# Kernel optimization log

Hardware: AMD Instinct MI355X
Metric: run time of the kernel (lower is better)

Reference implementation:

```python
import jax, jax.numpy as jnp
import numpy as np

B, CIN, COUT, H, W = 4, 256, 64, 64, 64


def setup_inputs() -> dict:
    key = jax.random.key(0)
    ks = jax.random.split(key, 9)
    s_in = 1.0 / np.sqrt(CIN)
    s_out = 1.0 / np.sqrt(COUT)
    return {
        "x": jax.random.normal(ks[0], (B, CIN, H, W), dtype=jnp.float32),
        "wq": jax.random.uniform(ks[1], (COUT, CIN), jnp.float32, -s_in, s_in),
        "bq": jax.random.uniform(ks[2], (COUT,), jnp.float32, -s_in, s_in),
        "wk": jax.random.uniform(ks[3], (COUT, CIN), jnp.float32, -s_in, s_in),
        "bk": jax.random.uniform(ks[4], (COUT,), jnp.float32, -s_in, s_in),
        "wv": jax.random.uniform(ks[5], (COUT, CIN), jnp.float32, -s_in, s_in),
        "bv": jax.random.uniform(ks[6], (COUT,), jnp.float32, -s_in, s_in),
        "wo": jax.random.uniform(ks[7], (CIN, COUT), jnp.float32, -s_out, s_out),
        "bo": jax.random.uniform(ks[8], (CIN,), jnp.float32, -s_out, s_out),
    }


def reference(x, wq, bq, wk, bk, wv, bv, wo, bo):
    b, f, h, w = x.shape
    xf = x.reshape(b, f, h * w)  # [b, f, hw]
    # 1x1-conv projections (conv2d k=1 == channel-wise linear), flattened to [b, c, hw]
    q = jnp.einsum("bfd,cf->bcd", xf, wq) + bq[None, :, None]
    k = jnp.einsum("bfd,cf->bcd", xf, wk) + bk[None, :, None]
    v = jnp.einsum("bfd,cf->bcd", xf, wv) + bv[None, :, None]
    # full spatial correlation [b, hw, hw], contracting channels (einsum 'bcd,bef->bdf')
    correl = jnp.einsum("bcd,bce->bde", q, k)
    correl = jax.nn.softmax(correl, axis=-1)
    # value @ correl -> [b, c, hw]
    o = jnp.einsum("bcd,bde->bce", v, correl)
    o = o.reshape(b, -1, h, w)
    # output 1x1 conv back to in_channels
    out = jnp.einsum("bchw,fc->bfhw", o, wo) + bo[None, :, None, None]
    return out
```

## Files before the change

### kernel.cpp

```cpp
#include <hip/hip_runtime.h>
#include <hip/hip_bf16.h>

#define BB 4
#define CIN 256
#define CO 64
#define HW_ 4096
#define SPLIT_A 8
#define SPLIT_S 8
#define DCHUNK_A (HW_ / SPLIT_A)
#define ECHUNK_S (HW_ / SPLIT_S)

typedef __attribute__((ext_vector_type(8))) short short8;
typedef __attribute__((ext_vector_type(4))) float f32x4;
typedef __attribute__((ext_vector_type(16))) float f32x16;
typedef __attribute__((ext_vector_type(4))) unsigned uint4v;
typedef __attribute__((ext_vector_type(2))) unsigned uint2v;

__device__ inline unsigned short f2bf(float f) {
  union { float f; unsigned u; } x; x.f = f;
  unsigned r = x.u + 0x7fffu + ((x.u >> 16) & 1u);
  return (unsigned short)(r >> 16);
}
__device__ inline float bf2f(unsigned short h) {
  union { unsigned u; float f; } x; x.u = ((unsigned)h) << 16;
  return x.f;
}
__device__ inline unsigned packbf2(float a, float b) {
  __hip_bfloat162 t = __float22bfloat162_rn(float2{a, b});
  union { __hip_bfloat162 h; unsigned u; } c; c.h = t; return c.u;
}
__device__ inline void gl_lds16(const void* g, void* l) {
  __builtin_amdgcn_global_load_lds(
      (const __attribute__((address_space(1))) unsigned int*)g,
      (__attribute__((address_space(3))) unsigned int*)l, 16, 0, 0);
}

__global__ __launch_bounds__(256, 3) void qkv_kernel(
    const float* __restrict__ x,
    const float* __restrict__ wq, const float* __restrict__ bq,
    const float* __restrict__ wk, const float* __restrict__ bk,
    const float* __restrict__ wv, const float* __restrict__ bv,
    unsigned short* __restrict__ qT, unsigned short* __restrict__ kT,
    unsigned short* __restrict__ v)
{
  const int b = blockIdx.z;
  const int which = blockIdx.y;
  const int n0 = blockIdx.x * 64;
  const int tid = threadIdx.x;
  const int w = tid >> 6, lane = tid & 63;
  const int lq = lane & 15, quad = lane >> 4;

  const float* W  = (which == 0) ? wq : (which == 1) ? wk : wv;
  const float* Bb = (which == 0) ? bq : (which == 1) ? bk : bv;

  __shared__ unsigned short w_lds[64 * 256];
  unsigned char* wbytes = reinterpret_cast<unsigned char*>(w_lds);

#pragma unroll
  for (int i = 0; i < 16; ++i) {
    int L = i * 256 + tid;
    int row = L >> 6, col4 = L & 63;
    float4 w4 = *reinterpret_cast<const float4*>(&W[row * 256 + col4 * 4]);
    ushort4 p;
    p.x = f2bf(w4.x); p.y = f2bf(w4.y); p.z = f2bf(w4.z); p.w = f2bf(w4.w);
    int addr = (row * 512 + col4 * 8) ^ ((row & 7) << 4);
    *reinterpret_cast<ushort4*>(wbytes + addr) = p;
  }
  __syncthreads();

  const int n = n0 + w * 16 + lq;
  const float* xb = x + (size_t)b * CIN * HW_ + n;

  const f32x4 zero = {0.f, 0.f, 0.f, 0.f};
  f32x4 acc[4];
#pragma unroll
  for (int mt = 0; mt < 4; ++mt) acc[mt] = zero;

  for (int ks = 0; ks < 8; ++ks) {
    float xv[8];
#pragma unroll
    for (int j = 0; j < 8; ++j)
      xv[j] = xb[(size_t)(ks * 32 + quad * 8 + j) * HW_];
    short8 bhi, blo;
#pragma unroll
    for (int j = 0; j < 8; ++j) {
      unsigned short h = f2bf(xv[j]);
      bhi[j] = (short)h;
      blo[j] = (short)f2bf(xv[j] - bf2f(h));
    }
#pragma unroll
    for (int mt = 0; mt < 4; ++mt) {
      int addr = ((mt * 16 + lq) * 512 + ks * 64 + quad * 16) ^ ((lq & 7) << 4);
      short8 af = *reinterpret_cast<const short8*>(wbytes + addr);
      acc[mt] = __builtin_amdgcn_mfma_f32_16x16x32_bf16(af, bhi, acc[mt], 0, 0, 0);
      acc[mt] = __builtin_amdgcn_mfma_f32_16x16x32_bf16(af, blo, acc[mt], 0, 0, 0);
    }
  }

  float4 bias4[4];
#pragma unroll
  for (int mt = 0; mt < 4; ++mt)
    bias4[mt] = *reinterpret_cast<const float4*>(&Bb[mt * 16 + quad * 4]);

  if (which < 2) {
    unsigned short* outp = ((which == 0) ? qT : kT) + ((size_t)b * HW_ + n) * 64;
#pragma unroll
    for (int mt = 0; mt < 4; ++mt) {
      ushort4 p;
      p.x = f2bf(acc[mt][0] + bias4[mt].x);
      p.y = f2bf(acc[mt][1] + bias4[mt].y);
      p.z = f2bf(acc[mt][2] + bias4[mt].z);
      p.w = f2bf(acc[mt][3] + bias4[mt].w);
      *reinterpret_cast<ushort4*>(&outp[mt * 16 + quad * 4]) = p;
    }
  } else {
#pragma unroll
    for (int mt = 0; mt < 4; ++mt) {
      float bb[4] = {bias4[mt].x, bias4[mt].y, bias4[mt].z, bias4[mt].w};
#pragma unroll
      for (int r = 0; r < 4; ++r)
        v[((size_t)b * CO + mt * 16 + quad * 4 + r) * HW_ + n] = f2bf(acc[mt][r] + bb[r]);
    }
  }
}

__global__ __launch_bounds__(256, 3) void stats_kernel(
    const unsigned short* __restrict__ qT,
    const unsigned short* __restrict__ kT,
    float2* __restrict__ parts)
{
  const int id = blockIdx.x;
  const int sw = (id & 7) * 128 + (id >> 3);
  const int dtile = sw & 31;
  const int esplit = (sw >> 5) & 7;
  const int b = sw >> 8;
  const int tid = threadIdx.x;
  const int w = tid >> 6, lane = tid & 63;
  const int lo = lane & 31, h = lane >> 5;

  __shared__ __align__(16) unsigned char k_lds[128 * 128];

  const size_t base = (size_t)b * HW_ * CO;
  const int d0 = dtile * 128 + w * 32;

  short8 qf[4];
#pragma unroll
  for (int ks = 0; ks < 4; ++ks)
    qf[ks] = *reinterpret_cast<const short8*>(&qT[base + (size_t)(d0 + lo) * 64 + ks * 16 + h * 8]);

  float m_run = -3.0e38f, l_run = 0.f;
  const char* kT_bytes = reinterpret_cast<const char*>(kT) + base * 2;
  const int e_beg = esplit * ECHUNK_S;

  for (int eb = e_beg; eb < e_beg + ECHUNK_S; eb += 128) {
#pragma unroll
    for (int j = 0; j < 4; ++j) {
      int chunk = w * 4 + j;
      int row = chunk * 8 + (lane >> 3);
      int cp = (lane & 7) * 16;
      gl_lds16(kT_bytes + (size_t)(eb + row) * 128 + (cp ^ ((row & 7) << 4)),
               k_lds + chunk * 1024);
    }
    __syncthreads();

#pragma unroll
    for (int et = 0; et < 4; ++et) {
      const int er = et * 32 + lo;
      f32x16 T;
#pragma unroll
      for (int i = 0; i < 16; ++i) T[i] = 0.f;
#pragma unroll
      for (int ks = 0; ks < 4; ++ks) {
        const short8 kfr = *reinterpret_cast<const short8*>(
            k_lds + er * 128 + ((ks * 32 + h * 16) ^ ((er & 7) << 4)));
        T = __builtin_amdgcn_mfma_f32_32x32x16_bf16(kfr, qf[ks], T, 0, 0, 0);
      }
      float tmax = T[0];
#pragma unroll
      for (int r = 1; r < 16; ++r) tmax = fmaxf(tmax, T[r]);
      tmax = fmaxf(tmax, __shfl_xor(tmax, 32));
      float m_new = fmaxf(m_run, tmax);
      float lsum = 0.f;
#pragma unroll
      for (int r = 0; r < 16; ++r) lsum += __expf(T[r] - m_new);
      lsum += __shfl_xor(lsum, 32);
      l_run = l_run * __expf(m_run - m_new) + lsum;
      m_run = m_new;
    }
    __syncthreads();
  }
  if (h == 0)
    parts[((size_t)b * HW_ + d0 + lo) * SPLIT_S + esplit] = make_float2(m_run, l_run);
}

__global__ __launch_bounds__(256) void combine_kernel(
    const float2* __restrict__ parts, float* __restrict__ ml)
{
  const int r = blockIdx.x * 256 + threadIdx.x;
  float2 p[SPLIT_S];
#pragma unroll
  for (int i = 0; i < SPLIT_S; ++i) p[i] = parts[(size_t)r * SPLIT_S + i];
  float M = p[0].x;
#pragma unroll
  for (int i = 1; i < SPLIT_S; ++i) M = fmaxf(M, p[i].x);
  float L = 0.f;
#pragma unroll
  for (int i = 0; i < SPLIT_S; ++i) L += p[i].y * __expf(p[i].x - M);
  ml[r] = M + __logf(L);
}

__global__ __launch_bounds__(256, 3) void apply_kernel(
    const unsigned short* __restrict__ qT,
    const unsigned short* __restrict__ kT,
    const unsigned short* __restrict__ vv,
    const float* __restrict__ ml,
    unsigned short* __restrict__ Opart)
{
  const int id = blockIdx.x;
  const int sw = (id & 7) * 128 + (id >> 3);
  const int et = sw & 31;
  const int split = (sw >> 5) & 7;
  const int b = sw >> 8;
  const int tid = threadIdx.x;
  const int w = tid >> 6, lane = tid & 63;
  const int lo = lane & 31, h = lane >> 5;

  __shared__ __align__(16) unsigned char q_lds[128 * 128];
  __shared__ __align__(16) unsigned char v_lds[64 * 256];

  const size_t base = (size_t)b * HW_ * CO;
  const int e0 = et * 128;
  const int e = e0 + w * 32 + lo;

  short8 kf[4];
#pragma unroll
  for (int ks = 0; ks < 4; ++ks)
    kf[ks] = *reinterpret_cast<const short8*>(&kT[base + (size_t)e * 64 + ks * 16 + h * 8]);

  f32x16 Of0, Of1;
#pragma unroll
  for (int i = 0; i < 16; ++i) { Of0[i] = 0.f; Of1[i] = 0.f; }

  const char* qT_bytes = reinterpret_cast<const char*>(qT) + base * 2;
  const char* v_bytes = reinterpret_cast<const char*>(vv) + base * 2;
  const float* mlb = ml + (size_t)b * HW_;

  const int d_beg = split * DCHUNK_A;
  for (int dt = d_beg; dt < d_beg + DCHUNK_A; dt += 128) {
#pragma unroll
    for (int j = 0; j < 4; ++j) {
      int chunk = w * 4 + j;
      {
        int row = chunk * 8 + (lane >> 3);
        int cp = (lane & 7) * 16;
        gl_lds16(qT_bytes + (size_t)(dt + row) * 128 + (cp ^ ((row & 7) << 4)),
                 q_lds + chunk * 1024);
      }
      {
        int vrow = chunk * 4 + (lane >> 4);
        int cp = (lane & 15) * 16;
        gl_lds16(v_bytes + (size_t)vrow * 8192 + dt * 2 + (cp ^ ((vrow & 15) << 4)),
                 v_lds + chunk * 1024);
      }
    }
    __syncthreads();

#pragma unroll
    for (int nt = 0; nt < 4; ++nt) {
      const int db = dt + nt * 32;
      const int lrow = nt * 32 + lo;
      f32x16 T;
#pragma unroll
      for (int i = 0; i < 16; ++i) T[i] = 0.f;
#pragma unroll
      for (int ks = 0; ks < 4; ++ks) {
        const short8 qfr = *reinterpret_cast<const short8*>(
            q_lds + lrow * 128 + ((ks * 32 + h * 16) ^ ((lrow & 7) << 4)));
        T = __builtin_amdgcn_mfma_f32_32x32x16_bf16(qfr, kf[ks], T, 0, 0, 0);
      }
      float p[16];
#pragma unroll
      for (int q = 0; q < 4; ++q) {
        f32x4 m4 = *reinterpret_cast<const f32x4*>(&mlb[db + q * 8 + h * 4]);
#pragma unroll
        for (int r = 0; r < 4; ++r)
          p[q * 4 + r] = __expf(T[q * 4 + r] - m4[r]);
      }
      unsigned pk[8];
#pragma unroll
      for (int m = 0; m < 8; ++m) pk[m] = packbf2(p[2 * m], p[2 * m + 1]);
#pragma unroll
      for (int kk = 0; kk < 2; ++kk) {
        uint2v s0 = __builtin_amdgcn_permlane32_swap(pk[kk * 4 + 0], pk[kk * 4 + 2], false, false);
        uint2v s1 = __builtin_amdgcn_permlane32_swap(pk[kk * 4 + 1], pk[kk * 4 + 3], false, false);
        uint4v pw_;
        pw_[0] = s0[0]; pw_[1] = s1[0]; pw_[2] = s0[1]; pw_[3] = s1[1];
        const short8 pf = *reinterpret_cast<const short8*>(&pw_);
        const int dcol = (nt * 32 + kk * 16) * 2 + h * 16;
        {
          const int row = lo;
          const short8 vf = *reinterpret_cast<const short8*>(
              v_lds + row * 256 + (dcol ^ ((row & 15) << 4)));
          Of0 = __builtin_amdgcn_mfma_f32_32x32x16_bf16(vf, pf, Of0, 0, 0, 0);
        }
        {
          const int row = 32 + lo;
          const short8 vf = *reinterpret_cast<const short8*>(
              v_lds + row * 256 + (dcol ^ ((row & 15) << 4)));
          Of1 = __builtin_amdgcn_mfma_f32_32x32x16_bf16(vf, pf, Of1, 0, 0, 0);
        }
      }
    }
    __syncthreads();
  }

  unsigned short* o_lds = reinterpret_cast<unsigned short*>(q_lds);
#pragma unroll
  for (int reg = 0; reg < 16; ++reg) {
    int rr = (reg & 3) + 8 * (reg >> 2) + 4 * h;
    o_lds[rr * 128 + w * 32 + lo] = f2bf(Of0[reg]);
    o_lds[(32 + rr) * 128 + w * 32 + lo] = f2bf(Of1[reg]);
  }
  __syncthreads();
  {
    const int c = tid >> 4;
    const int ee = (tid & 15) * 8;
#pragma unroll
    for (int p = 0; p < 4; ++p) {
      int cc = p * 16 + c;
      f32x4 wv_ = *reinterpret_cast<const f32x4*>(&o_lds[cc * 128 + ee]);
      __builtin_nontemporal_store(wv_, reinterpret_cast<f32x4*>(
          &Opart[((size_t)(b * SPLIT_A + split) * CO + cc) * HW_ + e0 + ee]));
    }
  }
}

__global__ __launch_bounds__(256) void outproj_kernel(
    const unsigned short* __restrict__ Opart, const float* __restrict__ wo,
    const float* __restrict__ bo, float* __restrict__ out)
{
  const int b = blockIdx.z;
  const int fh = blockIdx.y;
  const int n0 = blockIdx.x * 64;
  const int tid = threadIdx.x;
  const int w = tid >> 6, lane = tid & 63;
  const int lq = lane & 15, quad = lane >> 4;

  __shared__ __align__(16) unsigned short whi_lds[128 * 64];
  __shared__ __align__(16) unsigned short wlo_lds[128 * 64];
  unsigned char* whb = reinterpret_cast<unsigned char*>(whi_lds);
  unsigned char* wlb = reinterpret_cast<unsigned char*>(wlo_lds);

#pragma unroll
  for (int i = 0; i < 8; ++i) {
    int L = i * 256 + tid;
    int row = L >> 4, col4 = L & 15;
    float4 w4 = *reinterpret_cast<const float4*>(&wo[(size_t)(fh * 128 + row) * 64 + col4 * 4]);
    ushort4 hi, lo;
    hi.x = f2bf(w4.x); lo.x = f2bf(w4.x - bf2f(hi.x));
    hi.y = f2bf(w4.y); lo.y = f2bf(w4.y - bf2f(hi.y));
    hi.z = f2bf(w4.z); lo.z = f2bf(w4.z - bf2f(hi.z));
    hi.w = f2bf(w4.w); lo.w = f2bf(w4.w - bf2f(hi.w));
    int addr = (row * 128 + col4 * 8) ^ ((row & 7) << 4);
    *reinterpret_cast<ushort4*>(whb + addr) = hi;
    *reinterpret_cast<ushort4*>(wlb + addr) = lo;
  }
  __syncthreads();

  const int n = n0 + w * 16 + lq;
  const unsigned short* Ob = Opart + (size_t)(b * SPLIT_A) * CO * HW_;

  f32x4 acc[8];
#pragma unroll
  for (int mt = 0; mt < 8; ++mt)
    acc[mt] = *reinterpret_cast<const f32x4*>(&bo[fh * 128 + mt * 16 + quad * 4]);

#pragma unroll
  for (int ks = 0; ks < 2; ++ks) {
    short8 afh[8], afl[8];
#pragma unroll
    for (int mt = 0; mt < 8; ++mt) {
      int row = mt * 16 + lq;
      int addr = (row * 128 + ks * 64 + quad * 16) ^ ((row & 7) << 4);
      afh[mt] = *reinterpret_cast<const short8*>(whb + addr);
      afl[mt] = *reinterpret_cast<const short8*>(wlb + addr);
    }
#pragma unroll
    for (int s = 0; s < SPLIT_A; ++s) {
      short8 bf;
#pragma unroll
      for (int j = 0; j < 8; ++j)
        bf[j] = (short)Ob[(size_t)(s * CO + ks * 32 + quad * 8 + j) * HW_ + n];
#pragma unroll
      for (int mt = 0; mt < 8; ++mt) {
        acc[mt] = __builtin_amdgcn_mfma_f32_16x16x32_bf16(afh[mt], bf, acc[mt], 0, 0, 0);
        acc[mt] = __builtin_amdgcn_mfma_f32_16x16x32_bf16(afl[mt], bf, acc[mt], 0, 0, 0);
      }
    }
  }

#pragma unroll
  for (int mt = 0; mt < 8; ++mt) {
    int f = fh * 128 + mt * 16 + quad * 4;
#pragma unroll
    for (int r = 0; r < 4; ++r)
      out[((size_t)b * CIN + f + r) * HW_ + n] = acc[mt][r];
  }
}

extern "C" void kernel_launch(void* const* d_in, const int* in_sizes, int n_in,
                              void* d_out, int out_size, void* d_ws, size_t ws_size,
                              hipStream_t stream) {
  const float* x  = (const float*)d_in[0];
  const float* wq = (const float*)d_in[1];
  const float* bq = (const float*)d_in[2];
  const float* wk = (const float*)d_in[3];
  const float* bk = (const float*)d_in[4];
  const float* wv = (const float*)d_in[5];
  const float* bv = (const float*)d_in[6];
  const float* wo = (const float*)d_in[7];
  const float* bo = (const float*)d_in[8];
  float* out = (float*)d_out;

  char* ws = (char*)d_ws;
  unsigned short* qT    = (unsigned short*)(ws);
  unsigned short* kT    = (unsigned short*)(ws + (2u << 20));
  unsigned short* v     = (unsigned short*)(ws + (4u << 20));
  unsigned short* Opart = (unsigned short*)(ws + (6u << 20));
  float* ml             = (float*)(ws + (23u << 20));
  float2* parts         = (float2*)(ws + (24u << 20));

  qkv_kernel<<<dim3(64, 3, 4), 256, 0, stream>>>(x, wq, bq, wk, bk, wv, bv, qT, kT, v);
  stats_kernel<<<dim3(1024), 256, 0, stream>>>(qT, kT, parts);
  combine_kernel<<<dim3(BB * HW_ / 256), 256, 0, stream>>>(parts, ml);
  apply_kernel<<<dim3(1024), 256, 0, stream>>>(qT, kT, v, ml, Opart);
  outproj_kernel<<<dim3(64, 2, 4), 256, 0, stream>>>(Opart, wo, bo, out);
}
```

Before: 79.72 us.

## Double-buffer K and Q/V LDS tiles in stats and apply kernels

Both the softmax-stats and apply kernels now use two 64-row LDS buffers instead of one 128-row tile. The next tile is staged with async global-to-LDS loads while the current tile feeds the MFMAs, so load latency can overlap compute. The price is twice as many loop iterations and barriers, a halved tile size, and the V layout and swizzle changing to 128-byte rows. Total LDS use stays the same, so occupancy should not change.

After: 75.62 us. 1.05x faster.

```diff
diff --git a/kernel.cpp b/kernel.cpp
--- a/kernel.cpp
+++ b/kernel.cpp
@@ -138,7 +138,7 @@
   const int w = tid >> 6, lane = tid & 63;
   const int lo = lane & 31, h = lane >> 5;
 
-  __shared__ __align__(16) unsigned char k_lds[128 * 128];
+  __shared__ __align__(16) unsigned char k_lds[2][8192];
 
   const size_t base = (size_t)b * HW_ * CO;
   const int d0 = dtile * 128 + w * 32;
@@ -151,20 +151,28 @@
   float m_run = -3.0e38f, l_run = 0.f;
   const char* kT_bytes = reinterpret_cast<const char*>(kT) + base * 2;
   const int e_beg = esplit * ECHUNK_S;
-
-  for (int eb = e_beg; eb < e_beg + ECHUNK_S; eb += 128) {
-#pragma unroll
-    for (int j = 0; j < 4; ++j) {
-      int chunk = w * 4 + j;
+  const int NT = ECHUNK_S / 64;
+
+  auto stage = [&](int t, int buf) {
+    const int eb = e_beg + t * 64;
+#pragma unroll
+    for (int j = 0; j < 2; ++j) {
+      int chunk = w * 2 + j;
       int row = chunk * 8 + (lane >> 3);
       int cp = (lane & 7) * 16;
       gl_lds16(kT_bytes + (size_t)(eb + row) * 128 + (cp ^ ((row & 7) << 4)),
-               k_lds + chunk * 1024);
-    }
-    __syncthreads();
-
-#pragma unroll
-    for (int et = 0; et < 4; ++et) {
+               k_lds[buf] + chunk * 1024);
+    }
+  };
+
+  stage(0, 0);
+  __syncthreads();
+
+  for (int t = 0; t < NT; ++t) {
+    if (t + 1 < NT) stage(t + 1, (t + 1) & 1);
+    const unsigned char* kb = k_lds[t & 1];
+#pragma unroll
+    for (int et = 0; et < 2; ++et) {
       const int er = et * 32 + lo;
       f32x16 T;
 #pragma unroll
@@ -172,7 +180,7 @@
 #pragma unroll
       for (int ks = 0; ks < 4; ++ks) {
         const short8 kfr = *reinterpret_cast<const short8*>(
-            k_lds + er * 128 + ((ks * 32 + h * 16) ^ ((er & 7) << 4)));
+            kb + er * 128 + ((ks * 32 + h * 16) ^ ((er & 7) << 4)));
         T = __builtin_amdgcn_mfma_f32_32x32x16_bf16(kfr, qf[ks], T, 0, 0, 0);
       }
       float tmax = T[0];
@@ -225,8 +233,7 @@
   const int w = tid >> 6, lane = tid & 63;
   const int lo = lane & 31, h = lane >> 5;
 
-  __shared__ __align__(16) unsigned char q_lds[128 * 128];
-  __shared__ __align__(16) unsigned char v_lds[64 * 256];
+  __shared__ __align__(16) unsigned char lds_all[32768];
 
   const size_t base = (size_t)b * HW_ * CO;
   const int e0 = et * 128;
@@ -246,27 +253,32 @@
   const float* mlb = ml + (size_t)b * HW_;
 
   const int d_beg = split * DCHUNK_A;
-  for (int dt = d_beg; dt < d_beg + DCHUNK_A; dt += 128) {
-#pragma unroll
-    for (int j = 0; j < 4; ++j) {
-      int chunk = w * 4 + j;
-      {
-        int row = chunk * 8 + (lane >> 3);
-        int cp = (lane & 7) * 16;
-        gl_lds16(qT_bytes + (size_t)(dt + row) * 128 + (cp ^ ((row & 7) << 4)),
-                 q_lds + chunk * 1024);
-      }
-      {
-        int vrow = chunk * 4 + (lane >> 4);
-        int cp = (lane & 15) * 16;
-        gl_lds16(v_bytes + (size_t)vrow * 8192 + dt * 2 + (cp ^ ((vrow & 15) << 4)),
-                 v_lds + chunk * 1024);
-      }
-    }
-    __syncthreads();
-
-#pragma unroll
-    for (int nt = 0; nt < 4; ++nt) {
+  const int NT = DCHUNK_A / 64;
+
+  auto stage = [&](int t, int buf) {
+    const int dt = d_beg + t * 64;
+#pragma unroll
+    for (int j = 0; j < 2; ++j) {
+      int chunk = w * 2 + j;
+      int row = chunk * 8 + (lane >> 3);
+      int cp = (lane & 7) * 16;
+      gl_lds16(qT_bytes + (size_t)(dt + row) * 128 + (cp ^ ((row & 7) << 4)),
+               lds_all + buf * 8192 + chunk * 1024);
+      gl_lds16(v_bytes + (size_t)row * 8192 + dt * 2 + (cp ^ ((row & 7) << 4)),
+               lds_all + 16384 + buf * 8192 + chunk * 1024);
+    }
+  };
+
+  stage(0, 0);
+  __syncthreads();
+
+  for (int t = 0; t < NT; ++t) {
+    if (t + 1 < NT) stage(t + 1, (t + 1) & 1);
+    const int dt = d_beg + t * 64;
+    const unsigned char* qb = lds_all + (t & 1) * 8192;
+    const unsigned char* vb = lds_all + 16384 + (t & 1) * 8192;
+#pragma unroll
+    for (int nt = 0; nt < 2; ++nt) {
       const int db = dt + nt * 32;
       const int lrow = nt * 32 + lo;
       f32x16 T;
@@ -275,7 +287,7 @@
 #pragma unroll
       for (int ks = 0; ks < 4; ++ks) {
         const short8 qfr = *reinterpret_cast<const short8*>(
-            q_lds + lrow * 128 + ((ks * 32 + h * 16) ^ ((lrow & 7) << 4)));
+            qb + lrow * 128 + ((ks * 32 + h * 16) ^ ((lrow & 7) << 4)));
         T = __builtin_amdgcn_mfma_f32_32x32x16_bf16(qfr, kf[ks], T, 0, 0, 0);
       }
       float p[16];
@@ -300,13 +312,13 @@
         {
           const int row = lo;
           const short8 vf = *reinterpret_cast<const short8*>(
-              v_lds + row * 256 + (dcol ^ ((row & 15) << 4)));
+              vb + row * 128 + (dcol ^ ((row & 7) << 4)));
           Of0 = __builtin_amdgcn_mfma_f32_32x32x16_bf16(vf, pf, Of0, 0, 0, 0);
         }
         {
           const int row = 32 + lo;
           const short8 vf = *reinterpret_cast<const short8*>(
-              v_lds + row * 256 + (dcol ^ ((row & 15) << 4)));
+              vb + row * 128 + (dcol ^ ((row & 7) << 4)));
           Of1 = __builtin_amdgcn_mfma_f32_32x32x16_bf16(vf, pf, Of1, 0, 0, 0);
         }
       }
@@ -314,7 +326,7 @@
     __syncthreads();
   }
 
-  unsigned short* o_lds = reinterpret_cast<unsigned short*>(q_lds);
+  unsigned short* o_lds = reinterpret_cast<unsigned short*>(lds_all);
 #pragma unroll
   for (int reg = 0; reg < 16; ++reg) {
     int rr = (reg & 3) + 8 * (reg >> 2) + 4 * h;
```
